# Performance work log

Hardware: AMD Instinct MI355X
Metric: run time of the kernel (lower is better)

## Reference

```python
import jax, jax.numpy as jnp
import numpy as np
import math

L, B = 1024, 256
SEQ_DIM, KMER_DIM, HID = 16, 256, 64
N_LAYERS = 2
IN_DIM = SEQ_DIM + KMER_DIM + 21  # 293


def _normalize(v, eps=1e-12):
    return v / jnp.maximum(jnp.linalg.norm(v, axis=-1, keepdims=True), eps)


def _nerf_rot(a, b, c):
    # rotation matrix with columns [bc, n x bc, n] from last three backbone points
    bc = _normalize(c - b)
    n = _normalize(jnp.cross(b - a, bc))
    return jnp.stack([bc, jnp.cross(n, bc), n], axis=-1)  # (..., 3, 3)


def pnerf(c_tilde, nfrag):
    # c_tilde: (3L, B, 3) SRF coordinates; parallelized natural extension of reference frame
    Ltot, batch = c_tilde.shape[0], c_tilde.shape[1]
    k = Ltot // nfrag
    # contiguous fragments of length k, folded into the batch dim: (k, nfrag*B, 3)
    x = c_tilde.reshape(nfrag, k, batch, 3).transpose(1, 0, 2, 3).reshape(k, nfrag * batch, 3)
    init = jnp.array([[-math.sqrt(0.5), math.sqrt(1.5), 0.0],
                      [-math.sqrt(2.0), 0.0, 0.0],
                      [0.0, 0.0, 0.0]], dtype=c_tilde.dtype)
    F = nfrag * batch
    carry0 = (jnp.broadcast_to(init[0], (F, 3)),
              jnp.broadcast_to(init[1], (F, 3)),
              jnp.broadcast_to(init[2], (F, 3)))

    def extend(carry, ct):
        a, b, c = carry
        R = _nerf_rot(a, b, c)                      # (F, 3, 3)
        d = c + jnp.einsum('fij,fj->fi', R, ct)     # (F, 3)
        return (b, c, d), d

    _, frag = jax.lax.scan(extend, carry0, x)        # (k, F, 3)
    frag = frag.reshape(k, nfrag, batch, 3).transpose(1, 0, 2, 3)  # (nfrag, k, B, 3)

    # assemble fragments sequentially; init frame is identity/origin so frag 0 passes through
    carryA = (jnp.broadcast_to(init[0], (batch, 3)),
              jnp.broadcast_to(init[1], (batch, 3)),
              jnp.broadcast_to(init[2], (batch, 3)))

    def assemble(carry, fr):
        a, b, c = carry
        R = _nerf_rot(a, b, c)                      # (B, 3, 3)
        y = c + jnp.einsum('bij,kbj->kbi', R, fr)   # (k, B, 3)
        return (y[-3], y[-2], y[-1]), y

    _, ys = jax.lax.scan(assemble, carryA, frag)     # (nfrag, k, B, 3)
    return ys.reshape(nfrag * k, batch, 3)


def setup_inputs() -> dict:
    key = jax.random.key(0)
    ks = jax.random.split(key, 12)
    s = 0.05
    return {
        'seq': jax.random.randint(ks[0], (L, B), 0, 20, dtype=jnp.int64),
        'kmer': jax.random.randint(ks[1], (L, B), 0, 22 ** 3, dtype=jnp.int64),
        'pssm': jax.random.uniform(ks[2], (L, B, 21), dtype=jnp.float32),
        'length': jax.random.randint(ks[3], (L,), 1, L, dtype=jnp.int64),
        'seq_embed': jax.random.normal(ks[4], (20, SEQ_DIM), dtype=jnp.float32) * s,
        'kmer_embed': jax.random.normal(ks[5], (22 ** 3, KMER_DIM), dtype=jnp.float32) * s,
        'W0': jax.random.normal(ks[6], (IN_DIM, HID), dtype=jnp.float32) * s,
        'b0': jnp.zeros((HID,), dtype=jnp.float32),
        'We': jax.random.normal(ks[7], (HID, HID), dtype=jnp.float32) * s,
        'be': jnp.zeros((HID,), dtype=jnp.float32),
        'W1': jax.random.normal(ks[8], (HID, 9), dtype=jnp.float32) * s,
        'b1': jnp.zeros((9,), dtype=jnp.float32),
    }


def reference(seq, kmer, pssm, length, seq_embed, kmer_embed, W0, b0, We, be, W1, b1):
    s = seq_embed[seq]                                   # (L, B, 16)
    km = kmer_embed[kmer]                                # (L, B, 256)
    h = jnp.concatenate([s, km, pssm], axis=2)           # (L, B, 293)
    h = h @ W0 + b0                                      # (L, B, 64)
    # torch list-multiplication shares the SAME Linear across the n_layers blocks
    for _ in range(N_LAYERS):
        h = jax.nn.relu(h @ We + be)                     # dropout is identity at eval
    srf = h @ W1 + b1                                    # (L, B, 9)
    Ld, Bd = srf.shape[0], srf.shape[1]
    srf = srf.reshape(Ld, Bd, 3, 3).transpose(0, 2, 1, 3).reshape(3 * Ld, Bd, 3)
    return pnerf(srf, int(math.sqrt(Ld)))
```

## Files before the change

kernel.cpp:

```cpp
#include <hip/hip_runtime.h>
#include <math.h>

typedef short bf16x8 __attribute__((ext_vector_type(8)));
typedef float f32x4  __attribute__((ext_vector_type(4)));

__device__ __forceinline__ unsigned short f2bf(float x) {
    unsigned int u = __float_as_uint(x);
    return (unsigned short)((u + 0x7FFFu + ((u >> 16) & 1u)) >> 16);
}
__device__ __forceinline__ float bf2f(unsigned short h) {
    return __uint_as_float(((unsigned int)h) << 16);
}
__device__ __forceinline__ void split2(float x, unsigned short& h, unsigned short& l) {
    h = f2bf(x);
    l = f2bf(x - bf2f(h));
}
__device__ __forceinline__ void split2t(float x, unsigned short& h, unsigned short& l) {
    unsigned int u = __float_as_uint(x);
    h = (unsigned short)(u >> 16);
    float r = x - __uint_as_float(u & 0xFFFF0000u);
    l = f2bf(r);
}

__device__ __forceinline__ int hsw(int row, int col) {
    return row * 72 + ((((col >> 3) ^ ((row >> 2) & 3)) << 3) | (col & 7));
}

__device__ __forceinline__ float inv_norm3(float x, float y, float z) {
    float d = fmaf(x, x, fmaf(y, y, z * z));
    return rsqrtf(fmaxf(d, 1e-24f));
}
__device__ __forceinline__ float3 f3sub(float3 a, float3 b) {
    return make_float3(a.x - b.x, a.y - b.y, a.z - b.z);
}
__device__ __forceinline__ float3 f3cross(float3 a, float3 b) {
    return make_float3(a.y * b.z - a.z * b.y,
                       a.z * b.x - a.x * b.z,
                       a.x * b.y - a.y * b.x);
}
__device__ __forceinline__ void nerf_frame(const float3& A, const float3& Bv,
                                           const float3& C, float3& bc,
                                           float3& n, float3& m3) {
    float3 w  = f3sub(C, Bv);
    float3 v  = f3sub(Bv, A);
    float3 cr = f3cross(v, w);
    float iw = inv_norm3(w.x, w.y, w.z);
    float ic = inv_norm3(cr.x, cr.y, cr.z);
    bc = make_float3(w.x * iw, w.y * iw, w.z * iw);
    n  = make_float3(cr.x * ic, cr.y * ic, cr.z * ic);
    m3 = f3cross(n, bc);
}
__device__ __forceinline__ float3 nerf_place(const float3& C, const float3& bc,
                                             const float3& m3, const float3& n,
                                             float tx, float ty, float tz) {
    return make_float3(
        fmaf(m3.x, ty, fmaf(bc.x, tx, fmaf(n.x, tz, C.x))),
        fmaf(m3.y, ty, fmaf(bc.y, tx, fmaf(n.y, tz, C.y))),
        fmaf(m3.z, ty, fmaf(bc.z, tx, fmaf(n.z, tz, C.z))));
}

struct KParams {
    const int* seq; const int* kmer; const float* pssm;
    const float* se; const float* emb;
    const float* W0; const float* b0; const float* We; const float* be;
    const float* W1; const float* b1;
    float* kmerT; float* seqT; float* srf_t; float* fragbuf;
    float4* frames; float* FPbuf; float* out;
    unsigned short *WeTH, *WeTL, *W0pTH, *W0pTL, *W1TH, *W1TL;
};

__global__ __launch_bounds__(256) void tables_kernel(KParams P) {
    const int tid = threadIdx.x;
    const int vb  = blockIdx.x;
    if (vb < 167) {
        const int lane = tid & 63;
        const int wv   = __builtin_amdgcn_readfirstlane(tid >> 6);
        const int q    = lane >> 4;
        const int c16  = lane & 15;
        const int r0   = vb * 64;
        const int n    = wv * 16 + c16;

        bf16x8 BH[8], BL[8];
        #pragma unroll
        for (int kt8 = 0; kt8 < 8; ++kt8)
            #pragma unroll
            for (int j = 0; j < 8; ++j) {
                float w = P.W0[(16 + kt8 * 32 + q * 8 + j) * 64 + n];
                unsigned short h, l; split2t(w, h, l);
                BH[kt8][j] = (short)h; BL[kt8][j] = (short)l;
            }
        f32x4 acc[4];
        #pragma unroll
        for (int t = 0; t < 4; ++t) acc[t] = (f32x4){0.f, 0.f, 0.f, 0.f};
        #pragma unroll
        for (int kt8 = 0; kt8 < 8; ++kt8) {
            #pragma unroll
            for (int t = 0; t < 4; ++t) {
                int rr = r0 + t * 16 + c16;
                if (rr > 10647) rr = 10647;
                const float* ap = P.emb + rr * 256 + kt8 * 32 + q * 8;
                float4 a0 = *(const float4*)ap;
                float4 a1 = *(const float4*)(ap + 4);
                bf16x8 ah, al;
                unsigned short h, l;
                split2t(a0.x, h, l); ah[0] = (short)h; al[0] = (short)l;
                split2t(a0.y, h, l); ah[1] = (short)h; al[1] = (short)l;
                split2t(a0.z, h, l); ah[2] = (short)h; al[2] = (short)l;
                split2t(a0.w, h, l); ah[3] = (short)h; al[3] = (short)l;
                split2t(a1.x, h, l); ah[4] = (short)h; al[4] = (short)l;
                split2t(a1.y, h, l); ah[5] = (short)h; al[5] = (short)l;
                split2t(a1.z, h, l); ah[6] = (short)h; al[6] = (short)l;
                split2t(a1.w, h, l); ah[7] = (short)h; al[7] = (short)l;
                acc[t] = __builtin_amdgcn_mfma_f32_16x16x32_bf16(ah, BH[kt8], acc[t], 0, 0, 0);
                acc[t] = __builtin_amdgcn_mfma_f32_16x16x32_bf16(al, BH[kt8], acc[t], 0, 0, 0);
                acc[t] = __builtin_amdgcn_mfma_f32_16x16x32_bf16(ah, BL[kt8], acc[t], 0, 0, 0);
            }
        }
        #pragma unroll
        for (int t = 0; t < 4; ++t)
            #pragma unroll
            for (int r = 0; r < 4; ++r) {
                int row = r0 + t * 16 + q * 4 + r;
                if (row < 10648) P.kmerT[row * 64 + n] = acc[t][r];
            }
    } else if (vb < 172) {
        int e = (vb - 167) * 256 + tid;
        int r = e >> 6, j = e & 63;
        float acc = P.b0[j];
        #pragma unroll
        for (int k = 0; k < 16; ++k)
            acc = fmaf(P.se[r * 16 + k], P.W0[k * 64 + j], acc);
        float cs = 0.f;
        #pragma unroll
        for (int c = 0; c < 21; ++c) cs += P.W0[(272 + c) * 64 + j];
        P.seqT[r * 64 + j] = acc + 0.5f * cs;
    } else {
        #pragma unroll
        for (int i = 0; i < 16; ++i) {
            int e = i * 256 + tid;
            int k = e >> 6, n = e & 63;
            unsigned short h, l; split2(P.We[k * 64 + n], h, l);
            P.WeTH[n * 64 + k] = h; P.WeTL[n * 64 + k] = l;
        }
        #pragma unroll
        for (int i = 0; i < 8; ++i) {
            int e = i * 256 + tid;
            int k = e >> 6, n = e & 63;
            float w = (k < 21) ? P.W0[(272 + k) * 64 + n] : 0.f;
            unsigned short h, l; split2(w, h, l);
            P.W0pTH[n * 32 + k] = h; P.W0pTL[n * 32 + k] = l;
        }
        #pragma unroll
        for (int i = 0; i < 4; ++i) {
            int e = i * 256 + tid;
            int k = e >> 4, c = e & 15;
            float w = (c < 9) ? P.W1[k * 9 + c] : 0.f;
            unsigned short h, l; split2(w, h, l);
            P.W1TH[c * 64 + k] = h; P.W1TL[c * 64 + k] = l;
        }
    }
}

__global__ __launch_bounds__(256, 4) void mlp_kernel(KParams P) {
    __shared__ __align__(16) unsigned char SMEM[36864];
    unsigned short* Hah = (unsigned short*)(SMEM);
    unsigned short* Hal = (unsigned short*)(SMEM + 9216);
    unsigned short* Hbh = (unsigned short*)(SMEM + 18432);
    unsigned short* Hbl = (unsigned short*)(SMEM + 27648);
    unsigned short (*Ph)[40] = (unsigned short (*)[40])(SMEM + 18432);
    unsigned short (*Pl)[40] = (unsigned short (*)[40])(SMEM + 18432 + 5120);

    const int tid  = threadIdx.x;
    const int lane = tid & 63;
    const int wv   = __builtin_amdgcn_readfirstlane(tid >> 6);
    const int q    = lane >> 4;
    const int c16  = lane & 15;
    const int m0   = blockIdx.x * 64;
    const int n    = wv * 16 + c16;

    const int myseq = P.seq[m0 + lane];
    const int mykm  = P.kmer[m0 + lane];
    float g[4][4];
    #pragma unroll
    for (int t = 0; t < 4; ++t)
        #pragma unroll
        for (int r = 0; r < 4; ++r) {
            int src = (t * 16 + q * 4 + r) << 2;
            int s  = __builtin_amdgcn_ds_bpermute(src, myseq);
            int km = __builtin_amdgcn_ds_bpermute(src, mykm);
            g[t][r] = P.seqT[s * 64 + n] + P.kmerT[km * 64 + n];
        }

    for (int i = tid; i < 64 * 21; i += 256) {
        float v = P.pssm[m0 * 21 + i] - 0.5f;
        unsigned short h, l; split2t(v, h, l);
        Ph[i / 21][i % 21] = h;
        Pl[i / 21][i % 21] = l;
    }
    for (int i = tid; i < 64 * 11; i += 256) {
        Ph[i / 11][21 + (i % 11)] = 0;
        Pl[i / 11][21 + (i % 11)] = 0;
    }

    bf16x8 WeH[2], WeL[2], W1H[2], W1L[2], W0H, W0L;
    #pragma unroll
    for (int kk = 0; kk < 2; ++kk) {
        WeH[kk] = *(const bf16x8*)(P.WeTH + n * 64 + kk * 32 + q * 8);
        WeL[kk] = *(const bf16x8*)(P.WeTL + n * 64 + kk * 32 + q * 8);
        W1H[kk] = *(const bf16x8*)(P.W1TH + c16 * 64 + kk * 32 + q * 8);
        W1L[kk] = *(const bf16x8*)(P.W1TL + c16 * 64 + kk * 32 + q * 8);
    }
    W0H = *(const bf16x8*)(P.W0pTH + n * 32 + q * 8);
    W0L = *(const bf16x8*)(P.W0pTL + n * 32 + q * 8);
    const float be_n = P.be[n];
    const float b1h  = (c16 < 9) ? P.b1[c16] : 0.f;
    __syncthreads();

    f32x4 acc[4];
    #pragma unroll
    for (int t = 0; t < 4; ++t) acc[t] = (f32x4){0.f, 0.f, 0.f, 0.f};
    #pragma unroll
    for (int t = 0; t < 4; ++t) {
        bf16x8 ah = *(const bf16x8*)&Ph[t * 16 + c16][q * 8];
        bf16x8 al = *(const bf16x8*)&Pl[t * 16 + c16][q * 8];
        acc[t] = __builtin_amdgcn_mfma_f32_16x16x32_bf16(ah, W0H, acc[t], 0, 0, 0);
        acc[t] = __builtin_amdgcn_mfma_f32_16x16x32_bf16(al, W0H, acc[t], 0, 0, 0);
        acc[t] = __builtin_amdgcn_mfma_f32_16x16x32_bf16(ah, W0L, acc[t], 0, 0, 0);
    }
    #pragma unroll
    for (int t = 0; t < 4; ++t)
        #pragma unroll
        for (int r = 0; r < 4; ++r) {
            unsigned short h, l; split2t(acc[t][r] + g[t][r], h, l);
            Hah[hsw(t * 16 + q * 4 + r, n)] = h;
            Hal[hsw(t * 16 + q * 4 + r, n)] = l;
        }
    __syncthreads();

    {
        f32x4 a1[4];
        #pragma unroll
        for (int t = 0; t < 4; ++t) {
            a1[t] = (f32x4){be_n, be_n, be_n, be_n};
            #pragma unroll
            for (int kk = 0; kk < 2; ++kk) {
                bf16x8 ah = *(const bf16x8*)&Hah[hsw(t * 16 + c16, kk * 32 + q * 8)];
                bf16x8 al = *(const bf16x8*)&Hal[hsw(t * 16 + c16, kk * 32 + q * 8)];
                a1[t] = __builtin_amdgcn_mfma_f32_16x16x32_bf16(ah, WeH[kk], a1[t], 0, 0, 0);
                a1[t] = __builtin_amdgcn_mfma_f32_16x16x32_bf16(al, WeH[kk], a1[t], 0, 0, 0);
                a1[t] = __builtin_amdgcn_mfma_f32_16x16x32_bf16(ah, WeL[kk], a1[t], 0, 0, 0);
            }
        }
        #pragma unroll
        for (int t = 0; t < 4; ++t)
            #pragma unroll
            for (int r = 0; r < 4; ++r) {
                unsigned short h, l; split2t(fmaxf(a1[t][r], 0.f), h, l);
                Hbh[hsw(t * 16 + q * 4 + r, n)] = h;
                Hbl[hsw(t * 16 + q * 4 + r, n)] = l;
            }
        __syncthreads();
    }
    {
        f32x4 a2[4];
        #pragma unroll
        for (int t = 0; t < 4; ++t) {
            a2[t] = (f32x4){be_n, be_n, be_n, be_n};
            #pragma unroll
            for (int kk = 0; kk < 2; ++kk) {
                bf16x8 ah = *(const bf16x8*)&Hbh[hsw(t * 16 + c16, kk * 32 + q * 8)];
                bf16x8 al = *(const bf16x8*)&Hbl[hsw(t * 16 + c16, kk * 32 + q * 8)];
                a2[t] = __builtin_amdgcn_mfma_f32_16x16x32_bf16(ah, WeH[kk], a2[t], 0, 0, 0);
                a2[t] = __builtin_amdgcn_mfma_f32_16x16x32_bf16(al, WeH[kk], a2[t], 0, 0, 0);
                a2[t] = __builtin_amdgcn_mfma_f32_16x16x32_bf16(ah, WeL[kk], a2[t], 0, 0, 0);
            }
        }
        #pragma unroll
        for (int t = 0; t < 4; ++t)
            #pragma unroll
            for (int r = 0; r < 4; ++r) {
                unsigned short h, l; split2t(fmaxf(a2[t][r], 0.f), h, l);
                Hah[hsw(t * 16 + q * 4 + r, n)] = h;
                Hal[hsw(t * 16 + q * 4 + r, n)] = l;
            }
        __syncthreads();
    }
    {
        f32x4 ah4 = (f32x4){b1h, b1h, b1h, b1h};
        #pragma unroll
        for (int kk = 0; kk < 2; ++kk) {
            bf16x8 ah = *(const bf16x8*)&Hah[hsw(wv * 16 + c16, kk * 32 + q * 8)];
            bf16x8 al = *(const bf16x8*)&Hal[hsw(wv * 16 + c16, kk * 32 + q * 8)];
            ah4 = __builtin_amdgcn_mfma_f32_16x16x32_bf16(ah, W1H[kk], ah4, 0, 0, 0);
            ah4 = __builtin_amdgcn_mfma_f32_16x16x32_bf16(al, W1H[kk], ah4, 0, 0, 0);
            ah4 = __builtin_amdgcn_mfma_f32_16x16x32_bf16(ah, W1L[kk], ah4, 0, 0, 0);
        }
        if (c16 < 9) {
            #pragma unroll
            for (int r = 0; r < 4; ++r) {
                int pos = m0 + wv * 16 + q * 4 + r;
                int l = pos >> 8, b = pos & 255;
                P.srf_t[(l * 9 + c16) * 256 + b] = ah4[r];
            }
        }
    }
}

__global__ __launch_bounds__(64) void extend_kernel(KParams P) {
    int frag = blockIdx.x >> 2;
    int bb   = ((blockIdx.x & 3) << 6) + threadIdx.x;

    float3 A  = make_float3(-0.70710678118654752f, 1.22474487139158905f, 0.f);
    float3 Bv = make_float3(-1.41421356237309505f, 0.f, 0.f);
    float3 C  = make_float3(0.f, 0.f, 0.f);

    float ct0[9], ct1[9], ct2[9], ct3[9];
    #pragma unroll
    for (int m = 0; m < 9; ++m) {
        ct0[m] = P.srf_t[((frag * 32 + 0) * 9 + m) * 256 + bb];
        ct1[m] = P.srf_t[((frag * 32 + 1) * 9 + m) * 256 + bb];
        ct2[m] = P.srf_t[((frag * 32 + 2) * 9 + m) * 256 + bb];
    }
    for (int ll = 0; ll < 32; ++ll) {
        if (ll < 29) {
            #pragma unroll
            for (int m = 0; m < 9; ++m)
                ct3[m] = P.srf_t[((frag * 32 + ll + 3) * 9 + m) * 256 + bb];
        } else {
            #pragma unroll
            for (int m = 0; m < 9; ++m) ct3[m] = 0.f;
        }
        #pragma unroll
        for (int s3 = 0; s3 < 3; ++s3) {
            float3 bc, nn, m3;
            nerf_frame(A, Bv, C, bc, nn, m3);
            float3 d = nerf_place(C, bc, m3, nn,
                                  ct0[3 * s3 + 0], ct0[3 * s3 + 1], ct0[3 * s3 + 2]);
            int row = frag * 96 + ll * 3 + s3;
            P.fragbuf[(row * 3 + 0) * 256 + bb] = d.x;
            P.fragbuf[(row * 3 + 1) * 256 + bb] = d.y;
            P.fragbuf[(row * 3 + 2) * 256 + bb] = d.z;
            A = Bv; Bv = C; C = d;
        }
        #pragma unroll
        for (int m = 0; m < 9; ++m) { ct0[m] = ct1[m]; ct1[m] = ct2[m]; ct2[m] = ct3[m]; }
    }
    float3 bc, nn, m3;
    nerf_frame(A, Bv, C, bc, nn, m3);
    P.FPbuf[(frag * 12 + 0)  * 256 + bb] = bc.x;
    P.FPbuf[(frag * 12 + 1)  * 256 + bb] = bc.y;
    P.FPbuf[(frag * 12 + 2)  * 256 + bb] = bc.z;
    P.FPbuf[(frag * 12 + 3)  * 256 + bb] = m3.x;
    P.FPbuf[(frag * 12 + 4)  * 256 + bb] = m3.y;
    P.FPbuf[(frag * 12 + 5)  * 256 + bb] = m3.z;
    P.FPbuf[(frag * 12 + 6)  * 256 + bb] = nn.x;
    P.FPbuf[(frag * 12 + 7)  * 256 + bb] = nn.y;
    P.FPbuf[(frag * 12 + 8)  * 256 + bb] = nn.z;
    P.FPbuf[(frag * 12 + 9)  * 256 + bb] = C.x;
    P.FPbuf[(frag * 12 + 10) * 256 + bb] = C.y;
    P.FPbuf[(frag * 12 + 11) * 256 + bb] = C.z;
}

__global__ __launch_bounds__(256) void carry_kernel(KParams P) {
    __shared__ float S[384][16];
    const int tid  = threadIdx.x;
    const int base = blockIdx.x * 16;
    for (int i = tid; i < 384 * 16; i += 256) {
        int row = i >> 4, col = i & 15;
        S[row][col] = P.FPbuf[row * 256 + base + col];
    }
    __syncthreads();
    if (tid < 16) {
        int bb = base + tid;
        float3 ob = make_float3(1.f, 0.f, 0.f);
        float3 om = make_float3(0.f, 1.f, 0.f);
        float3 on = make_float3(0.f, 0.f, 1.f);
        float3 c  = make_float3(0.f, 0.f, 0.f);
        for (int f = 0; f < 32; ++f) {
            int fb = (f * 256 + bb) * 3;
            P.frames[fb + 0] = make_float4(ob.x, ob.y, ob.z, om.x);
            P.frames[fb + 1] = make_float4(om.y, om.z, on.x, on.y);
            P.frames[fb + 2] = make_float4(on.z, c.x, c.y, c.z);

            int r0 = f * 12;
            float3 Fb = make_float3(S[r0+0][tid], S[r0+1][tid], S[r0+2][tid]);
            float3 Fm = make_float3(S[r0+3][tid], S[r0+4][tid], S[r0+5][tid]);
            float3 Fn = make_float3(S[r0+6][tid], S[r0+7][tid], S[r0+8][tid]);
            float3 p  = make_float3(S[r0+9][tid], S[r0+10][tid], S[r0+11][tid]);

            float3 nb = make_float3(
                fmaf(ob.x,Fb.x, fmaf(om.x,Fb.y, on.x*Fb.z)),
                fmaf(ob.y,Fb.x, fmaf(om.y,Fb.y, on.y*Fb.z)),
                fmaf(ob.z,Fb.x, fmaf(om.z,Fb.y, on.z*Fb.z)));
            float3 nm = make_float3(
                fmaf(ob.x,Fm.x, fmaf(om.x,Fm.y, on.x*Fm.z)),
                fmaf(ob.y,Fm.x, fmaf(om.y,Fm.y, on.y*Fm.z)),
                fmaf(ob.z,Fm.x, fmaf(om.z,Fm.y, on.z*Fm.z)));
            float3 nn2 = make_float3(
                fmaf(ob.x,Fn.x, fmaf(om.x,Fn.y, on.x*Fn.z)),
                fmaf(ob.y,Fn.x, fmaf(om.y,Fn.y, on.y*Fn.z)),
                fmaf(ob.z,Fn.x, fmaf(om.z,Fn.y, on.z*Fn.z)));
            float3 nc = make_float3(
                fmaf(ob.x,p.x, fmaf(om.x,p.y, fmaf(on.x,p.z, c.x))),
                fmaf(ob.y,p.x, fmaf(om.y,p.y, fmaf(on.y,p.z, c.y))),
                fmaf(ob.z,p.x, fmaf(om.z,p.y, fmaf(on.z,p.z, c.z))));
            ob = nb; om = nm; on = nn2; c = nc;
        }
    }
}

__global__ __launch_bounds__(256) void apply_kernel(KParams P) {
    __shared__ float sm[768];
    const int bb = threadIdx.x;
    #pragma unroll 1
    for (int i = 0; i < 4; ++i) {
        const int row  = blockIdx.x * 4 + i;
        const int frag = row / 96;

        float fx = P.fragbuf[(row * 3 + 0) * 256 + bb];
        float fy = P.fragbuf[(row * 3 + 1) * 256 + bb];
        float fz = P.fragbuf[(row * 3 + 2) * 256 + bb];

        int fb = (frag * 256 + bb) * 3;
        float4 f0 = P.frames[fb + 0];
        float4 f1 = P.frames[fb + 1];
        float4 f2 = P.frames[fb + 2];

        float ox = f2.y + f0.x * fx + f0.w * fy + f1.z * fz;
        float oy = f2.z + f0.y * fx + f1.x * fy + f1.w * fz;
        float oz = f2.w + f0.z * fx + f1.y * fy + f2.x * fz;

        __syncthreads();
        sm[bb * 3 + 0] = ox;
        sm[bb * 3 + 1] = oy;
        sm[bb * 3 + 2] = oz;
        __syncthreads();

        int base = row * 768;
        P.out[base + bb]       = sm[bb];
        P.out[base + 256 + bb] = sm[256 + bb];
        P.out[base + 512 + bb] = sm[512 + bb];
    }
}

extern "C" void kernel_launch(void* const* d_in, const int* in_sizes, int n_in,
                              void* d_out, int out_size, void* d_ws, size_t ws_size,
                              hipStream_t stream) {
    float* ws      = (float*)d_ws;
    float* kmerT   = ws;
    float* seqT    = kmerT + 681472;
    float* srf_t   = seqT + 1280;
    float* fragbuf = srf_t + 2359296;
    float* frames  = fragbuf + 2359296;
    float* FPbuf   = frames + 98304;

    unsigned short* WeTH  = (unsigned short*)fragbuf;
    unsigned short* WeTL  = WeTH + 4096;
    unsigned short* W0pTH = WeTL + 4096;
    unsigned short* W0pTL = W0pTH + 2048;
    unsigned short* W1TH  = W0pTL + 2048;
    unsigned short* W1TL  = W1TH + 1024;

    KParams P;
    P.seq  = (const int*)d_in[0];
    P.kmer = (const int*)d_in[1];
    P.pssm = (const float*)d_in[2];
    P.se   = (const float*)d_in[4];
    P.emb  = (const float*)d_in[5];
    P.W0   = (const float*)d_in[6];
    P.b0   = (const float*)d_in[7];
    P.We   = (const float*)d_in[8];
    P.be   = (const float*)d_in[9];
    P.W1   = (const float*)d_in[10];
    P.b1   = (const float*)d_in[11];
    P.kmerT = kmerT; P.seqT = seqT; P.srf_t = srf_t; P.fragbuf = fragbuf;
    P.frames = (float4*)frames; P.FPbuf = FPbuf; P.out = (float*)d_out;
    P.WeTH = WeTH; P.WeTL = WeTL; P.W0pTH = W0pTH; P.W0pTL = W0pTL;
    P.W1TH = W1TH; P.W1TL = W1TL;

    hipLaunchKernelGGL(tables_kernel, dim3(173),  dim3(256), 0, stream, P);
    hipLaunchKernelGGL(mlp_kernel,    dim3(4096), dim3(256), 0, stream, P);
    hipLaunchKernelGGL(extend_kernel, dim3(128),  dim3(64),  0, stream, P);
    hipLaunchKernelGGL(carry_kernel,  dim3(16),   dim3(256), 0, stream, P);
    hipLaunchKernelGGL(apply_kernel,  dim3(768),  dim3(256), 0, stream, P);
}
```

Before: 176.2 us.

## Give each wave its own 16-row tile so MLP layers need no block barriers

The MLP kernel is reorganised so that each wavefront owns 16 rows and computes all 64 output columns, instead of four waves splitting the columns of a shared 64-row tile. Each wave's hidden activations now live in its own LDS slice, which removes every __syncthreads between layers. It also drops the ds_bpermute index shuffles, since each lane loads its own seq and kmer indices. In exchange, each wave keeps all the We weight fragments in registers (four times as many bf16x8 values), which raises VGPR pressure and may limit occupancy.

```diff
diff --git a/kernel.cpp b/kernel.cpp
--- a/kernel.cpp
+++ b/kernel.cpp
@@ -162,145 +162,164 @@
 }
 
 __global__ __launch_bounds__(256, 4) void mlp_kernel(KParams P) {
-    __shared__ __align__(16) unsigned char SMEM[36864];
-    unsigned short* Hah = (unsigned short*)(SMEM);
-    unsigned short* Hal = (unsigned short*)(SMEM + 9216);
-    unsigned short* Hbh = (unsigned short*)(SMEM + 18432);
-    unsigned short* Hbl = (unsigned short*)(SMEM + 27648);
-    unsigned short (*Ph)[40] = (unsigned short (*)[40])(SMEM + 18432);
-    unsigned short (*Pl)[40] = (unsigned short (*)[40])(SMEM + 18432 + 5120);
+    __shared__ __align__(16) unsigned short Hbuf[2][4][2][16][72];
 
     const int tid  = threadIdx.x;
     const int lane = tid & 63;
     const int wv   = __builtin_amdgcn_readfirstlane(tid >> 6);
     const int q    = lane >> 4;
     const int c16  = lane & 15;
-    const int m0   = blockIdx.x * 64;
-    const int n    = wv * 16 + c16;
-
-    const int myseq = P.seq[m0 + lane];
-    const int mykm  = P.kmer[m0 + lane];
+    const int m0s  = blockIdx.x * 64 + wv * 16;
+
+    unsigned short (*Ah)[72] = Hbuf[0][wv][0];
+    unsigned short (*Al)[72] = Hbuf[0][wv][1];
+    unsigned short (*Bh)[72] = Hbuf[1][wv][0];
+    unsigned short (*Bl)[72] = Hbuf[1][wv][1];
+    unsigned short (*Ph)[40] = (unsigned short (*)[40])&Bh[0][0];
+    unsigned short (*Pl)[40] = (unsigned short (*)[40])&Bl[0][0];
+
+    int sidx[4], kidx[4];
+    #pragma unroll
+    for (int r = 0; r < 4; ++r) {
+        sidx[r] = P.seq[m0s + q * 4 + r];
+        kidx[r] = P.kmer[m0s + q * 4 + r];
+    }
     float g[4][4];
     #pragma unroll
-    for (int t = 0; t < 4; ++t)
-        #pragma unroll
-        for (int r = 0; r < 4; ++r) {
-            int src = (t * 16 + q * 4 + r) << 2;
-            int s  = __builtin_amdgcn_ds_bpermute(src, myseq);
-            int km = __builtin_amdgcn_ds_bpermute(src, mykm);
-            g[t][r] = P.seqT[s * 64 + n] + P.kmerT[km * 64 + n];
-        }
-
-    for (int i = tid; i < 64 * 21; i += 256) {
-        float v = P.pssm[m0 * 21 + i] - 0.5f;
+    for (int nt = 0; nt < 4; ++nt)
+        #pragma unroll
+        for (int r = 0; r < 4; ++r)
+            g[nt][r] = P.seqT[sidx[r] * 64 + nt * 16 + c16]
+                     + P.kmerT[kidx[r] * 64 + nt * 16 + c16];
+
+    for (int i = lane; i < 16 * 21; i += 64) {
+        float v = P.pssm[(m0s + i / 21) * 21 + i % 21] - 0.5f;
         unsigned short h, l; split2t(v, h, l);
         Ph[i / 21][i % 21] = h;
         Pl[i / 21][i % 21] = l;
     }
-    for (int i = tid; i < 64 * 11; i += 256) {
+    for (int i = lane; i < 16 * 11; i += 64) {
         Ph[i / 11][21 + (i % 11)] = 0;
         Pl[i / 11][21 + (i % 11)] = 0;
     }
 
-    bf16x8 WeH[2], WeL[2], W1H[2], W1L[2], W0H, W0L;
+    f32x4 acc[4];
+    {
+        bf16x8 W0H[4], W0L[4];
+        #pragma unroll
+        for (int nt = 0; nt < 4; ++nt) {
+            W0H[nt] = *(const bf16x8*)(P.W0pTH + (nt * 16 + c16) * 32 + q * 8);
+            W0L[nt] = *(const bf16x8*)(P.W0pTL + (nt * 16 + c16) * 32 + q * 8);
+        }
+        bf16x8 pah = *(const bf16x8*)&Ph[c16][q * 8];
+        bf16x8 pal = *(const bf16x8*)&Pl[c16][q * 8];
+        #pragma unroll
+        for (int nt = 0; nt < 4; ++nt) {
+            acc[nt] = (f32x4){0.f, 0.f, 0.f, 0.f};
+            acc[nt] = __builtin_amdgcn_mfma_f32_16x16x32_bf16(pah, W0H[nt], acc[nt], 0, 0, 0);
+            acc[nt] = __builtin_amdgcn_mfma_f32_16x16x32_bf16(pal, W0H[nt], acc[nt], 0, 0, 0);
+            acc[nt] = __builtin_amdgcn_mfma_f32_16x16x32_bf16(pah, W0L[nt], acc[nt], 0, 0, 0);
+        }
+    }
     #pragma unroll
-    for (int kk = 0; kk < 2; ++kk) {
-        WeH[kk] = *(const bf16x8*)(P.WeTH + n * 64 + kk * 32 + q * 8);
-        WeL[kk] = *(const bf16x8*)(P.WeTL + n * 64 + kk * 32 + q * 8);
-        W1H[kk] = *(const bf16x8*)(P.W1TH + c16 * 64 + kk * 32 + q * 8);
-        W1L[kk] = *(const bf16x8*)(P.W1TL + c16 * 64 + kk * 32 + q * 8);
-    }
-    W0H = *(const bf16x8*)(P.W0pTH + n * 32 + q * 8);
-    W0L = *(const bf16x8*)(P.W0pTL + n * 32 + q * 8);
-    const float be_n = P.be[n];
-    const float b1h  = (c16 < 9) ? P.b1[c16] : 0.f;
-    __syncthreads();
-
-    f32x4 acc[4];
+    for (int nt = 0; nt < 4; ++nt)
+        #pragma unroll
+        for (int r = 0; r < 4; ++r) {
+            unsigned short h, l; split2t(acc[nt][r] + g[nt][r], h, l);
+            int idx = hsw(q * 4 + r, nt * 16 + c16);
+            (&Ah[0][0])[idx] = h;
+            (&Al[0][0])[idx] = l;
+        }
+
+    bf16x8 WeH[4][2], WeL[4][2];
     #pragma unroll
-    for (int t = 0; t < 4; ++t) acc[t] = (f32x4){0.f, 0.f, 0.f, 0.f};
+    for (int nt = 0; nt < 4; ++nt)
+        #pragma unroll
+        for (int kk = 0; kk < 2; ++kk) {
+            WeH[nt][kk] = *(const bf16x8*)(P.WeTH + (nt * 16 + c16) * 64 + kk * 32 + q * 8);
+            WeL[nt][kk] = *(const bf16x8*)(P.WeTL + (nt * 16 + c16) * 64 + kk * 32 + q * 8);
+        }
+    float bias[4];
     #pragma unroll
-    for (int t = 0; t < 4; ++t) {
-        bf16x8 ah = *(const bf16x8*)&Ph[t * 16 + c16][q * 8];
-        bf16x8 al = *(const bf16x8*)&Pl[t * 16 + c16][q * 8];
-        acc[t] = __builtin_amdgcn_mfma_f32_16x16x32_bf16(ah, W0H, acc[t], 0, 0, 0);
-        acc[t] = __builtin_amdgcn_mfma_f32_16x16x32_bf16(al, W0H, acc[t], 0, 0, 0);
-        acc[t] = __builtin_amdgcn_mfma_f32_16x16x32_bf16(ah, W0L, acc[t], 0, 0, 0);
-    }
-    #pragma unroll
-    for (int t = 0; t < 4; ++t)
-        #pragma unroll
-        for (int r = 0; r < 4; ++r) {
-            unsigned short h, l; split2t(acc[t][r] + g[t][r], h, l);
-            Hah[hsw(t * 16 + q * 4 + r, n)] = h;
-            Hal[hsw(t * 16 + q * 4 + r, n)] = l;
-        }
-    __syncthreads();
+    for (int nt = 0; nt < 4; ++nt) bias[nt] = P.be[nt * 16 + c16];
 
     {
-        f32x4 a1[4];
-        #pragma unroll
-        for (int t = 0; t < 4; ++t) {
-            a1[t] = (f32x4){be_n, be_n, be_n, be_n};
-            #pragma unroll
-            for (int kk = 0; kk < 2; ++kk) {
-                bf16x8 ah = *(const bf16x8*)&Hah[hsw(t * 16 + c16, kk * 32 + q * 8)];
-                bf16x8 al = *(const bf16x8*)&Hal[hsw(t * 16 + c16, kk * 32 + q * 8)];
-                a1[t] = __builtin_amdgcn_mfma_f32_16x16x32_bf16(ah, WeH[kk], a1[t], 0, 0, 0);
-                a1[t] = __builtin_amdgcn_mfma_f32_16x16x32_bf16(al, WeH[kk], a1[t], 0, 0, 0);
-                a1[t] = __builtin_amdgcn_mfma_f32_16x16x32_bf16(ah, WeL[kk], a1[t], 0, 0, 0);
+        bf16x8 a0h = *(const bf16x8*)&(&Ah[0][0])[hsw(c16, q * 8)];
+        bf16x8 a0l = *(const bf16x8*)&(&Al[0][0])[hsw(c16, q * 8)];
+        bf16x8 a1h = *(const bf16x8*)&(&Ah[0][0])[hsw(c16, 32 + q * 8)];
+        bf16x8 a1l = *(const bf16x8*)&(&Al[0][0])[hsw(c16, 32 + q * 8)];
+        #pragma unroll
+        for (int nt = 0; nt < 4; ++nt) {
+            f32x4 a = (f32x4){bias[nt], bias[nt], bias[nt], bias[nt]};
+            a = __builtin_amdgcn_mfma_f32_16x16x32_bf16(a0h, WeH[nt][0], a, 0, 0, 0);
+            a = __builtin_amdgcn_mfma_f32_16x16x32_bf16(a0l, WeH[nt][0], a, 0, 0, 0);
+            a = __builtin_amdgcn_mfma_f32_16x16x32_bf16(a0h, WeL[nt][0], a, 0, 0, 0);
+            a = __builtin_amdgcn_mfma_f32_16x16x32_bf16(a1h, WeH[nt][1], a, 0, 0, 0);
+            a = __builtin_amdgcn_mfma_f32_16x16x32_bf16(a1l, WeH[nt][1], a, 0, 0, 0);
+            a = __builtin_amdgcn_mfma_f32_16x16x32_bf16(a1h, WeL[nt][1], a, 0, 0, 0);
+            acc[nt] = (f32x4){fmaxf(a[0], 0.f), fmaxf(a[1], 0.f),
+                              fmaxf(a[2], 0.f), fmaxf(a[3], 0.f)};
+        }
+        #pragma unroll
+        for (int nt = 0; nt < 4; ++nt)
+            #pragma unroll
+            for (int r = 0; r < 4; ++r) {
+                unsigned short h, l; split2t(acc[nt][r], h, l);
+                int idx = hsw(q * 4 + r, nt * 16 + c16);
+                (&Bh[0][0])[idx] = h;
+                (&Bl[0][0])[idx] = l;
             }
-        }
-        #pragma unroll
-        for (int t = 0; t < 4; ++t)
+    }
+    {
+        bf16x8 a0h = *(const bf16x8*)&(&Bh[0][0])[hsw(c16, q * 8)];
+        bf16x8 a0l = *(const bf16x8*)&(&Bl[0][0])[hsw(c16, q * 8)];
+        bf16x8 a1h = *(const bf16x8*)&(&Bh[0][0])[hsw(c16, 32 + q * 8)];
+        bf16x8 a1l = *(const bf16x8*)&(&Bl[0][0])[hsw(c16, 32 + q * 8)];
+        #pragma unroll
+        for (int nt = 0; nt < 4; ++nt) {
+            f32x4 a = (f32x4){bias[nt], bias[nt], bias[nt], bias[nt]};
+            a = __builtin_amdgcn_mfma_f32_16x16x32_bf16(a0h, WeH[nt][0], a, 0, 0, 0);
+            a = __builtin_amdgcn_mfma_f32_16x16x32_bf16(a0l, WeH[nt][0], a, 0, 0, 0);
+            a = __builtin_amdgcn_mfma_f32_16x16x32_bf16(a0h, WeL[nt][0], a, 0, 0, 0);
+            a = __builtin_amdgcn_mfma_f32_16x16x32_bf16(a1h, WeH[nt][1], a, 0, 0, 0);
+            a = __builtin_amdgcn_mfma_f32_16x16x32_bf16(a1l, WeH[nt][1], a, 0, 0, 0);
+            a = __builtin_amdgcn_mfma_f32_16x16x32_bf16(a1h, WeL[nt][1], a, 0, 0, 0);
+            acc[nt] = (f32x4){fmaxf(a[0], 0.f), fmaxf(a[1], 0.f),
+                              fmaxf(a[2], 0.f), fmaxf(a[3], 0.f)};
+        }
+        #pragma unroll
+        for (int nt = 0; nt < 4; ++nt)
             #pragma unroll
             for (int r = 0; r < 4; ++r) {
-                unsigned short h, l; split2t(fmaxf(a1[t][r], 0.f), h, l);
-                Hbh[hsw(t * 16 + q * 4 + r, n)] = h;
-                Hbl[hsw(t * 16 + q * 4 + r, n)] = l;
+                unsigned short h, l; split2t(acc[nt][r], h, l);
+                int idx = hsw(q * 4 + r, nt * 16 + c16);
+                (&Ah[0][0])[idx] = h;
+                (&Al[0][0])[idx] = l;
             }
-        __syncthreads();
     }
     {
-        f32x4 a2[4];
-        #pragma unroll
-        for (int t = 0; t < 4; ++t) {
-            a2[t] = (f32x4){be_n, be_n, be_n, be_n};
-            #pragma unroll
-            for (int kk = 0; kk < 2; ++kk) {
-                bf16x8 ah = *(const bf16x8*)&Hbh[hsw(t * 16 + c16, kk * 32 + q * 8)];
-                bf16x8 al = *(const bf16x8*)&Hbl[hsw(t * 16 + c16, kk * 32 + q * 8)];
-                a2[t] = __builtin_amdgcn_mfma_f32_16x16x32_bf16(ah, WeH[kk], a2[t], 0, 0, 0);
-                a2[t] = __builtin_amdgcn_mfma_f32_16x16x32_bf16(al, WeH[kk], a2[t], 0, 0, 0);
-                a2[t] = __builtin_amdgcn_mfma_f32_16x16x32_bf16(ah, WeL[kk], a2[t], 0, 0, 0);
-            }
-        }
-        #pragma unroll
-        for (int t = 0; t < 4; ++t)
+        bf16x8 a0h = *(const bf16x8*)&(&Ah[0][0])[hsw(c16, q * 8)];
+        bf16x8 a0l = *(const bf16x8*)&(&Al[0][0])[hsw(c16, q * 8)];
+        bf16x8 a1h = *(const bf16x8*)&(&Ah[0][0])[hsw(c16, 32 + q * 8)];
+        bf16x8 a1l = *(const bf16x8*)&(&Al[0][0])[hsw(c16, 32 + q * 8)];
+        bf16x8 W1H0 = *(const bf16x8*)(P.W1TH + c16 * 64 + q * 8);
+        bf16x8 W1L0 = *(const bf16x8*)(P.W1TL + c16 * 64 + q * 8);
+        bf16x8 W1H1 = *(const bf16x8*)(P.W1TH + c16 * 64 + 32 + q * 8);
+        bf16x8 W1L1 = *(const bf16x8*)(P.W1TL + c16 * 64 + 32 + q * 8);
+        float b1h = (c16 < 9) ? P.b1[c16] : 0.f;
+        f32x4 a = (f32x4){b1h, b1h, b1h, b1h};
+        a = __builtin_amdgcn_mfma_f32_16x16x32_bf16(a0h, W1H0, a, 0, 0, 0);
+        a = __builtin_amdgcn_mfma_f32_16x16x32_bf16(a0l, W1H0, a, 0, 0, 0);
+        a = __builtin_amdgcn_mfma_f32_16x16x32_bf16(a0h, W1L0, a, 0, 0, 0);
+        a = __builtin_amdgcn_mfma_f32_16x16x32_bf16(a1h, W1H1, a, 0, 0, 0);
+        a = __builtin_amdgcn_mfma_f32_16x16x32_bf16(a1l, W1H1, a, 0, 0, 0);
+        a = __builtin_amdgcn_mfma_f32_16x16x32_bf16(a1h, W1L1, a, 0, 0, 0);
+        if (c16 < 9) {
             #pragma unroll
             for (int r = 0; r < 4; ++r) {
-                unsigned short h, l; split2t(fmaxf(a2[t][r], 0.f), h, l);
-                Hah[hsw(t * 16 + q * 4 + r, n)] = h;
-                Hal[hsw(t * 16 + q * 4 + r, n)] = l;
-            }
-        __syncthreads();
-    }
-    {
-        f32x4 ah4 = (f32x4){b1h, b1h, b1h, b1h};
-        #pragma unroll
-        for (int kk = 0; kk < 2; ++kk) {
-            bf16x8 ah = *(const bf16x8*)&Hah[hsw(wv * 16 + c16, kk * 32 + q * 8)];
-            bf16x8 al = *(const bf16x8*)&Hal[hsw(wv * 16 + c16, kk * 32 + q * 8)];
-            ah4 = __builtin_amdgcn_mfma_f32_16x16x32_bf16(ah, W1H[kk], ah4, 0, 0, 0);
-            ah4 = __builtin_amdgcn_mfma_f32_16x16x32_bf16(al, W1H[kk], ah4, 0, 0, 0);
-            ah4 = __builtin_amdgcn_mfma_f32_16x16x32_bf16(ah, W1L[kk], ah4, 0, 0, 0);
-        }
-        if (c16 < 9) {
-            #pragma unroll
-            for (int r = 0; r < 4; ++r) {
-                int pos = m0 + wv * 16 + q * 4 + r;
+                int pos = m0s + q * 4 + r;
                 int l = pos >> 8, b = pos & 255;
-                P.srf_t[(l * 9 + c16) * 256 + b] = ah4[r];
+                P.srf_t[(l * 9 + c16) * 256 + b] = a[r];
             }
         }
     }
```

Result: slower. 194.5 us (+10.4%).

## Fuse fragment carry into apply kernel by recomputing frame prefix per block

Applied to the files above, without the earlier changes.

Removes the separate serial carry kernel, which ran on only 16 threads per block, along with its frames buffer. Each apply block now recomputes the composed fragment frame for its own fragment by walking the per-fragment frame parameters from FPbuf, prefetching the next step's values. This saves one launch and a dependent serial kernel, at the cost of redundant recomputation of up to 31 frame compositions per block and more global reads of FPbuf, which should mostly hit in cache.

```diff
diff --git a/kernel.cpp b/kernel.cpp
--- a/kernel.cpp
+++ b/kernel.cpp
@@ -65,7 +65,7 @@
     const float* W0; const float* b0; const float* We; const float* be;
     const float* W1; const float* b1;
     float* kmerT; float* seqT; float* srf_t; float* fragbuf;
-    float4* frames; float* FPbuf; float* out;
+    float* FPbuf; float* out;
     unsigned short *WeTH, *WeTL, *W0pTH, *W0pTL, *W1TH, *W1TL;
 };
 
@@ -361,32 +361,34 @@
     P.FPbuf[(frag * 12 + 11) * 256 + bb] = C.z;
 }
 
-__global__ __launch_bounds__(256) void carry_kernel(KParams P) {
-    __shared__ float S[384][16];
-    const int tid  = threadIdx.x;
-    const int base = blockIdx.x * 16;
-    for (int i = tid; i < 384 * 16; i += 256) {
-        int row = i >> 4, col = i & 15;
-        S[row][col] = P.FPbuf[row * 256 + base + col];
-    }
-    __syncthreads();
-    if (tid < 16) {
-        int bb = base + tid;
-        float3 ob = make_float3(1.f, 0.f, 0.f);
-        float3 om = make_float3(0.f, 1.f, 0.f);
-        float3 on = make_float3(0.f, 0.f, 1.f);
-        float3 c  = make_float3(0.f, 0.f, 0.f);
-        for (int f = 0; f < 32; ++f) {
-            int fb = (f * 256 + bb) * 3;
-            P.frames[fb + 0] = make_float4(ob.x, ob.y, ob.z, om.x);
-            P.frames[fb + 1] = make_float4(om.y, om.z, on.x, on.y);
-            P.frames[fb + 2] = make_float4(on.z, c.x, c.y, c.z);
-
-            int r0 = f * 12;
-            float3 Fb = make_float3(S[r0+0][tid], S[r0+1][tid], S[r0+2][tid]);
-            float3 Fm = make_float3(S[r0+3][tid], S[r0+4][tid], S[r0+5][tid]);
-            float3 Fn = make_float3(S[r0+6][tid], S[r0+7][tid], S[r0+8][tid]);
-            float3 p  = make_float3(S[r0+9][tid], S[r0+10][tid], S[r0+11][tid]);
+__global__ __launch_bounds__(256) void carry_apply_kernel(KParams P) {
+    const int bb   = threadIdx.x;
+    const int row0 = blockIdx.x * 4;
+    const int frag = row0 / 96;
+
+    float3 ob = make_float3(1.f, 0.f, 0.f);
+    float3 om = make_float3(0.f, 1.f, 0.f);
+    float3 on = make_float3(0.f, 0.f, 1.f);
+    float3 c  = make_float3(0.f, 0.f, 0.f);
+
+    if (frag > 0) {
+        float v[12];
+        #pragma unroll
+        for (int j = 0; j < 12; ++j) v[j] = P.FPbuf[j * 256 + bb];
+        for (int f = 0; f < frag; ++f) {
+            float nv[12];
+            if (f + 1 < frag) {
+                #pragma unroll
+                for (int j = 0; j < 12; ++j)
+                    nv[j] = P.FPbuf[((f + 1) * 12 + j) * 256 + bb];
+            } else {
+                #pragma unroll
+                for (int j = 0; j < 12; ++j) nv[j] = 0.f;
+            }
+            float3 Fb = make_float3(v[0], v[1], v[2]);
+            float3 Fm = make_float3(v[3], v[4], v[5]);
+            float3 Fn = make_float3(v[6], v[7], v[8]);
+            float3 p  = make_float3(v[9], v[10], v[11]);
 
             float3 nb = make_float3(
                 fmaf(ob.x,Fb.x, fmaf(om.x,Fb.y, on.x*Fb.z)),
@@ -405,30 +407,23 @@
                 fmaf(ob.y,p.x, fmaf(om.y,p.y, fmaf(on.y,p.z, c.y))),
                 fmaf(ob.z,p.x, fmaf(om.z,p.y, fmaf(on.z,p.z, c.z))));
             ob = nb; om = nm; on = nn2; c = nc;
-        }
-    }
-}
-
-__global__ __launch_bounds__(256) void apply_kernel(KParams P) {
+            #pragma unroll
+            for (int j = 0; j < 12; ++j) v[j] = nv[j];
+        }
+    }
+
     __shared__ float sm[768];
-    const int bb = threadIdx.x;
     #pragma unroll 1
     for (int i = 0; i < 4; ++i) {
-        const int row  = blockIdx.x * 4 + i;
-        const int frag = row / 96;
+        const int row = row0 + i;
 
         float fx = P.fragbuf[(row * 3 + 0) * 256 + bb];
         float fy = P.fragbuf[(row * 3 + 1) * 256 + bb];
         float fz = P.fragbuf[(row * 3 + 2) * 256 + bb];
 
-        int fb = (frag * 256 + bb) * 3;
-        float4 f0 = P.frames[fb + 0];
-        float4 f1 = P.frames[fb + 1];
-        float4 f2 = P.frames[fb + 2];
-
-        float ox = f2.y + f0.x * fx + f0.w * fy + f1.z * fz;
-        float oy = f2.z + f0.y * fx + f1.x * fy + f1.w * fz;
-        float oz = f2.w + f0.z * fx + f1.y * fy + f2.x * fz;
+        float ox = c.x + ob.x * fx + om.x * fy + on.x * fz;
+        float oy = c.y + ob.y * fx + om.y * fy + on.y * fz;
+        float oz = c.z + ob.z * fx + om.z * fy + on.z * fz;
 
         __syncthreads();
         sm[bb * 3 + 0] = ox;
@@ -451,8 +446,7 @@
     float* seqT    = kmerT + 681472;
     float* srf_t   = seqT + 1280;
     float* fragbuf = srf_t + 2359296;
-    float* frames  = fragbuf + 2359296;
-    float* FPbuf   = frames + 98304;
+    float* FPbuf   = fragbuf + 2359296;
 
     unsigned short* WeTH  = (unsigned short*)fragbuf;
     unsigned short* WeTL  = WeTH + 4096;
@@ -474,13 +468,12 @@
     P.W1   = (const float*)d_in[10];
     P.b1   = (const float*)d_in[11];
     P.kmerT = kmerT; P.seqT = seqT; P.srf_t = srf_t; P.fragbuf = fragbuf;
-    P.frames = (float4*)frames; P.FPbuf = FPbuf; P.out = (float*)d_out;
+    P.FPbuf = FPbuf; P.out = (float*)d_out;
     P.WeTH = WeTH; P.WeTL = WeTL; P.W0pTH = W0pTH; P.W0pTL = W0pTL;
     P.W1TH = W1TH; P.W1TL = W1TL;
 
-    hipLaunchKernelGGL(tables_kernel, dim3(173),  dim3(256), 0, stream, P);
-    hipLaunchKernelGGL(mlp_kernel,    dim3(4096), dim3(256), 0, stream, P);
-    hipLaunchKernelGGL(extend_kernel, dim3(128),  dim3(64),  0, stream, P);
-    hipLaunchKernelGGL(carry_kernel,  dim3(16),   dim3(256), 0, stream, P);
-    hipLaunchKernelGGL(apply_kernel,  dim3(768),  dim3(256), 0, stream, P);
-}
+    hipLaunchKernelGGL(tables_kernel,      dim3(173),  dim3(256), 0, stream, P);
+    hipLaunchKernelGGL(mlp_kernel,         dim3(4096), dim3(256), 0, stream, P);
+    hipLaunchKernelGGL(extend_kernel,      dim3(128),  dim3(64),  0, stream, P);
+    hipLaunchKernelGGL(carry_apply_kernel, dim3(768),  dim3(256), 0, stream, P);
+}
```

Result: slower. 180.8 us (+2.6%).
